# Kernel tuning notes

Measured on AMD Instinct MI355X. Metric: run time of the kernel, lower is better.

The kernel has to match this reference:

```python
import jax, jax.numpy as jnp
import numpy as np


def _unpack_int4(packed):
    """Unpack bytes (stored as int32 in [0,256)) into signed int4 values in [-8,7].
    packed: [..., K/2] -> [..., K], low nibble first."""
    lo = packed & 0xF
    hi = (packed >> 4) & 0xF
    lo = lo - 16 * (lo >= 8).astype(jnp.int32)
    hi = hi - 16 * (hi >= 8).astype(jnp.int32)
    out = jnp.stack([lo, hi], axis=-1)
    return out.reshape(packed.shape[:-1] + (packed.shape[-1] * 2,))


def setup_inputs() -> dict:
    key = jax.random.key(0)
    ks = jax.random.split(key, 7)
    M, K, N, R = 8192, 4096, 4096, 32
    return {
        "x_quant": jax.random.randint(ks[0], (M, K // 2), 0, 256, dtype=jnp.int32),
        "x_scale": jax.random.uniform(ks[1], (M,), dtype=jnp.float32) * 0.01 + 1e-3,
        "weight": jax.random.randint(ks[2], (N, K // 2), 0, 256, dtype=jnp.int32),
        "weight_scales": jax.random.uniform(ks[3], (N,), dtype=jnp.float32) * 0.01 + 1e-3,
        "bias": jax.random.normal(ks[4], (N,), dtype=jnp.float32) * 0.01,
        "x_r": jax.random.normal(ks[5], (M, R), dtype=jnp.float32),
        "w_outlier": jax.random.normal(ks[6], (N, R), dtype=jnp.float32),
    }


def reference(x_quant, x_scale, weight, weight_scales, bias, x_r, w_outlier):
    # Unpack packed int4 operands: [M,K] and [N,K], values in [-8,7]
    xq = _unpack_int4(x_quant)
    wq = _unpack_int4(weight)
    # Integer GEMM (s4s4 accumulate in int32), then fused dequant + bias
    acc = jnp.matmul(xq, wq.T)  # [M, N] int32
    out = acc.astype(jnp.float32) * x_scale[:, None] * weight_scales[None, :] + bias[None, :]
    # Low-rank outlier correction: addmm_(x_r, w_outlier.T)
    out = out + jnp.matmul(x_r, w_outlier.T)
    return out
```

## Files before the change

### kernel.cpp

```cpp
#include <hip/hip_runtime.h>

#define M_ 8192
#define K_ 4096
#define N_ 4096
#define R_ 32
#define KP_ (K_ / 2)

#define BM 256
#define BN 256
#define BK 64
#define NT (K_ / BK)
#define ATILE 16384
#define TILE_SZ 32768
#define GRID ((M_ / BM) * (N_ / BN))

typedef __attribute__((ext_vector_type(4))) int    i32x4;
typedef __attribute__((ext_vector_type(4))) float  f32x4;
typedef __attribute__((ext_vector_type(8))) __bf16 bf16x8;

__device__ __forceinline__ void gload16(const void* g, void* l) {
  __builtin_amdgcn_global_load_lds(
      (const __attribute__((address_space(1))) unsigned int*)g,
      (__attribute__((address_space(3))) unsigned int*)l, 16, 0, 0);
}

__device__ __forceinline__ unsigned nib2(int b) {
  unsigned lo = (unsigned)(((b & 15) ^ 8) - 8) & 0xFFu;
  unsigned hi = (unsigned)((((b >> 4) & 15) ^ 8) - 8) & 0xFFu;
  return lo | (hi << 8);
}

__global__ void repack_tiled(const int* __restrict__ in, uint4* __restrict__ out) {
  const int tile = blockIdx.x;
  const int rt = tile >> 6, kt = tile & 63;
  const int t = threadIdx.x;
  #pragma unroll
  for (int i = 0; i < 4; ++i) {
    int g = t + i * 256;
    int u = g >> 6, l = g & 63;
    int row = rt * 256 + u * 16 + (l & 15);
    int w0  = kt * 32 + (l >> 4) * 8;
    const int4* p = (const int4*)(in + (size_t)row * KP_ + w0);
    int4 a = p[0], b = p[1];
    uint4 o;
    o.x = nib2(a.x) | (nib2(a.y) << 16);
    o.y = nib2(a.z) | (nib2(a.w) << 16);
    o.z = nib2(b.x) | (nib2(b.y) << 16);
    o.w = nib2(b.z) | (nib2(b.w) << 16);
    out[(size_t)tile * 1024 + g] = o;
  }
}

__device__ __forceinline__ unsigned short f2b(float x) {
  unsigned u = __float_as_uint(x);
  return (unsigned short)((u + 0x7FFFu + ((u >> 16) & 1u)) >> 16);
}

__global__ void f2bf4(const float* __restrict__ in, unsigned short* __restrict__ out, int n4) {
  int stride = gridDim.x * blockDim.x;
  for (int i = blockIdx.x * blockDim.x + threadIdx.x; i < n4; i += stride) {
    float4 f = ((const float4*)in)[i];
    ushort4 o;
    o.x = f2b(f.x); o.y = f2b(f.y); o.z = f2b(f.z); o.w = f2b(f.w);
    ((ushort4*)out)[i] = o;
  }
}

__global__ __launch_bounds__(512, 2) void gemm_w4a4(
    const char* __restrict__ x8t, const char* __restrict__ w8t,
    const unsigned short* __restrict__ xrb, const unsigned short* __restrict__ wob,
    const float* __restrict__ xscale, const float* __restrict__ wscale,
    const float* __restrict__ bias, float* __restrict__ out)
{
  extern __shared__ __align__(16) char lds[];

  const int t    = threadIdx.x;
  const int w    = t >> 6;
  const int l    = t & 63;
  const int lrow = l & 15;
  const int lgrp = l >> 4;
  const int wr   = w >> 2;
  const int wc   = w & 3;

  const int swz = (blockIdx.x & 7) * (GRID / 8) + (blockIdx.x >> 3);
  const int mt  = swz & 31, nt = swz >> 5;
  const int m0  = mt * BM, n0 = nt * BN;

  const char* aT = x8t + (size_t)mt * NT * ATILE;
  const char* bT = w8t + (size_t)nt * NT * ATILE;

#define STAGE_A(tile)                                                         \
  { const char* s = aT + (size_t)(tile) * ATILE + w * 1024 + (l) * 16;        \
    char* d = lds + ((tile) & 3) * TILE_SZ + w * 1024;                        \
    gload16(s, d); gload16(s + 8192, d + 8192); }
#define STAGE_B(tile)                                                         \
  { const char* s = bT + (size_t)(tile) * ATILE + w * 1024 + (l) * 16;        \
    char* d = lds + ((tile) & 3) * TILE_SZ + ATILE + w * 1024;                \
    gload16(s, d); gload16(s + 8192, d + 8192); }
#define FENCE asm volatile("" ::: "memory")

  i32x4 acc[8][4] = {};

  STAGE_A(0) STAGE_B(0)
  STAGE_A(1) STAGE_B(1)
  STAGE_A(2) STAGE_B(2)
  asm volatile("s_waitcnt vmcnt(8)" ::: "memory");
  __builtin_amdgcn_s_barrier();
  FENCE;

  for (int kt = 0; kt < NT; ++kt) {
    const char* Ab = lds + (kt & 3) * TILE_SZ;
    const char* Bb = Ab + ATILE;

    i32x4 bf[4], af0[4];
    #pragma unroll
    for (int n = 0; n < 4; ++n)
      bf[n] = *(const i32x4*)(Bb + (wc * 4 + n) * 1024 + l * 16);
    #pragma unroll
    for (int m = 0; m < 4; ++m)
      af0[m] = *(const i32x4*)(Ab + (wr * 8 + m) * 1024 + l * 16);
    if (kt < NT - 3) STAGE_A(kt + 3)
    FENCE;
    __builtin_amdgcn_s_barrier();
    FENCE;
    __builtin_amdgcn_s_setprio(1);
    #pragma unroll
    for (int m = 0; m < 4; ++m)
      #pragma unroll
      for (int n = 0; n < 4; ++n)
        acc[m][n] = __builtin_amdgcn_mfma_i32_16x16x64_i8(af0[m], bf[n], acc[m][n], 0, 0, 0);
    __builtin_amdgcn_s_setprio(0);
    FENCE;
    __builtin_amdgcn_s_barrier();
    FENCE;

    i32x4 af1[4];
    #pragma unroll
    for (int m = 0; m < 4; ++m)
      af1[m] = *(const i32x4*)(Ab + (wr * 8 + 4 + m) * 1024 + l * 16);
    if (kt < NT - 3) {
      STAGE_B(kt + 3)
      asm volatile("s_waitcnt vmcnt(8)" ::: "memory");
    } else if (kt == NT - 3) {
      asm volatile("s_waitcnt vmcnt(4)" ::: "memory");
    } else if (kt == NT - 2) {
      asm volatile("s_waitcnt vmcnt(0)" ::: "memory");
    }
    FENCE;
    __builtin_amdgcn_s_barrier();
    FENCE;
    __builtin_amdgcn_s_setprio(1);
    #pragma unroll
    for (int m = 0; m < 4; ++m)
      #pragma unroll
      for (int n = 0; n < 4; ++n)
        acc[4 + m][n] = __builtin_amdgcn_mfma_i32_16x16x64_i8(af1[m], bf[n], acc[4 + m][n], 0, 0, 0);
    __builtin_amdgcn_s_setprio(0);
    FENCE;
    __builtin_amdgcn_s_barrier();
    FENCE;
  }

  f32x4 sxv[8];
  #pragma unroll
  for (int m = 0; m < 8; ++m)
    sxv[m] = *(const f32x4*)(xscale + m0 + wr * 128 + m * 16 + lgrp * 4);
  float swv[4], bv[4];
  #pragma unroll
  for (int n = 0; n < 4; ++n) {
    int cg = n0 + wc * 64 + n * 16 + lrow;
    swv[n] = wscale[cg];
    bv[n]  = bias[cg];
  }
  bf16x8 ar[8], br[4];
  #pragma unroll
  for (int m = 0; m < 8; ++m)
    ar[m] = *(const bf16x8*)(xrb + (size_t)(m0 + wr * 128 + m * 16 + lrow) * R_ + lgrp * 8);
  #pragma unroll
  for (int n = 0; n < 4; ++n)
    br[n] = *(const bf16x8*)(wob + (size_t)(n0 + wc * 64 + n * 16 + lrow) * R_ + lgrp * 8);

  #pragma unroll
  for (int m = 0; m < 8; ++m) {
    #pragma unroll
    for (int n = 0; n < 4; ++n) {
      f32x4 z = {0.0f, 0.0f, 0.0f, 0.0f};
      f32x4 c = __builtin_amdgcn_mfma_f32_16x16x32_bf16(ar[m], br[n], z, 0, 0, 0);
      #pragma unroll
      for (int j = 0; j < 4; ++j) {
        int rg = m0 + wr * 128 + m * 16 + lgrp * 4 + j;
        int cg = n0 + wc * 64 + n * 16 + lrow;
        out[(size_t)rg * N_ + cg] =
            (float)acc[m][n][j] * sxv[m][j] * swv[n] + c[j] + bv[n];
      }
    }
  }
}

extern "C" void kernel_launch(void* const* d_in, const int* in_sizes, int n_in,
                              void* d_out, int out_size, void* d_ws, size_t ws_size,
                              hipStream_t stream) {
  const int*   x_quant   = (const int*)d_in[0];
  const float* x_scale   = (const float*)d_in[1];
  const int*   weight    = (const int*)d_in[2];
  const float* w_scales  = (const float*)d_in[3];
  const float* bias      = (const float*)d_in[4];
  const float* x_r       = (const float*)d_in[5];
  const float* w_outlier = (const float*)d_in[6];
  float* out = (float*)d_out;

  char* ws = (char*)d_ws;
  char*           x8t = ws;
  char*           w8t = ws + (size_t)M_ * K_;
  unsigned short* xrb = (unsigned short*)(ws + (size_t)M_ * K_ + (size_t)N_ * K_);
  unsigned short* wob = xrb + (size_t)M_ * R_;

  (void)hipFuncSetAttribute((const void*)gemm_w4a4,
                            hipFuncAttributeMaxDynamicSharedMemorySize,
                            4 * TILE_SZ);

  repack_tiled<<<(M_ / BM) * NT, 256, 0, stream>>>(x_quant, (uint4*)x8t);
  repack_tiled<<<(N_ / BN) * NT, 256, 0, stream>>>(weight,  (uint4*)w8t);
  f2bf4<<<256, 256, 0, stream>>>(x_r, xrb, M_ * R_ / 4);
  f2bf4<<<128, 256, 0, stream>>>(w_outlier, wob, N_ * R_ / 4);

  gemm_w4a4<<<GRID, 512, 4 * TILE_SZ, stream>>>(
      x8t, w8t, xrb, wob, x_scale, w_scales, bias, out);
}
```

Baseline: 170.1 us.

## Switch int8 GEMM to 256x128 tiles with 32x32x32 MFMA and triple buffering

Reworks the GEMM: block tile shrinks from 256x256 to 256x128 with 4 waves instead of 8, each wave computing a 128x64 subtile using 32x32x32 int8 MFMAs in place of 16x16x64. The repack kernels are rewritten to produce a 32-row fragment layout that matches the new MFMA operand format, and the LDS pipeline moves from a 4-stage split A/B staging to a 3-buffer scheme with one barrier per k-step. The epilogue is adapted to the 32x32 accumulator layout. This doubles the grid and lowers per-block LDS use, which may help occupancy and cut barrier overhead, but it lowers data reuse per block and increases global traffic for A.

After: 202.5 us. 1.19x slower.

```diff
diff --git a/kernel.cpp b/kernel.cpp
--- a/kernel.cpp
+++ b/kernel.cpp
@@ -7,16 +7,19 @@
 #define KP_ (K_ / 2)
 
 #define BM 256
-#define BN 256
+#define BN 128
 #define BK 64
-#define NT (K_ / BK)
-#define ATILE 16384
-#define TILE_SZ 32768
+#define NT 64
+#define A_TILE 16384
+#define B_TILE 8192
+#define BUF_SZ (A_TILE + B_TILE)
 #define GRID ((M_ / BM) * (N_ / BN))
 
-typedef __attribute__((ext_vector_type(4))) int    i32x4;
-typedef __attribute__((ext_vector_type(4))) float  f32x4;
-typedef __attribute__((ext_vector_type(8))) __bf16 bf16x8;
+typedef __attribute__((ext_vector_type(4)))  int    i32x4;
+typedef __attribute__((ext_vector_type(16))) int    i32x16;
+typedef __attribute__((ext_vector_type(4)))  float  f32x4;
+typedef __attribute__((ext_vector_type(16))) float  f32x16;
+typedef __attribute__((ext_vector_type(8)))  __bf16 bf16x8;
 
 __device__ __forceinline__ void gload16(const void* g, void* l) {
   __builtin_amdgcn_global_load_lds(
@@ -30,25 +33,38 @@
   return lo | (hi << 8);
 }
 
-__global__ void repack_tiled(const int* __restrict__ in, uint4* __restrict__ out) {
-  const int tile = blockIdx.x;
-  const int rt = tile >> 6, kt = tile & 63;
-  const int t = threadIdx.x;
-  #pragma unroll
-  for (int i = 0; i < 4; ++i) {
-    int g = t + i * 256;
-    int u = g >> 6, l = g & 63;
-    int row = rt * 256 + u * 16 + (l & 15);
-    int w0  = kt * 32 + (l >> 4) * 8;
-    const int4* p = (const int4*)(in + (size_t)row * KP_ + w0);
-    int4 a = p[0], b = p[1];
-    uint4 o;
-    o.x = nib2(a.x) | (nib2(a.y) << 16);
-    o.y = nib2(a.z) | (nib2(a.w) << 16);
-    o.z = nib2(b.x) | (nib2(b.y) << 16);
-    o.w = nib2(b.z) | (nib2(b.w) << 16);
-    out[(size_t)tile * 1024 + g] = o;
-  }
+__global__ void repack_a(const int* __restrict__ in, uint4* __restrict__ out) {
+  int i = blockIdx.x * 256 + threadIdx.x;
+  int l = i & 63;
+  int u = (i >> 6) & 15;
+  int tile = i >> 10;
+  int row = (tile >> 6) * 256 + (u >> 1) * 32 + (l & 31);
+  int w0  = (tile & 63) * 32 + (u & 1) * 16 + (l >> 5) * 8;
+  const int4* p = (const int4*)(in + (size_t)row * KP_ + w0);
+  int4 a = p[0], b = p[1];
+  uint4 o;
+  o.x = nib2(a.x) | (nib2(a.y) << 16);
+  o.y = nib2(a.z) | (nib2(a.w) << 16);
+  o.z = nib2(b.x) | (nib2(b.y) << 16);
+  o.w = nib2(b.z) | (nib2(b.w) << 16);
+  out[i] = o;
+}
+
+__global__ void repack_b(const int* __restrict__ in, uint4* __restrict__ out) {
+  int i = blockIdx.x * 256 + threadIdx.x;
+  int l = i & 63;
+  int u = (i >> 6) & 7;
+  int tile = i >> 9;
+  int row = (tile >> 6) * 128 + (u >> 1) * 32 + (l & 31);
+  int w0  = (tile & 63) * 32 + (u & 1) * 16 + (l >> 5) * 8;
+  const int4* p = (const int4*)(in + (size_t)row * KP_ + w0);
+  int4 a = p[0], b = p[1];
+  uint4 o;
+  o.x = nib2(a.x) | (nib2(a.y) << 16);
+  o.y = nib2(a.z) | (nib2(a.w) << 16);
+  o.z = nib2(b.x) | (nib2(b.y) << 16);
+  o.w = nib2(b.z) | (nib2(b.w) << 16);
+  out[i] = o;
 }
 
 __device__ __forceinline__ unsigned short f2b(float x) {
@@ -66,132 +82,123 @@
   }
 }
 
-__global__ __launch_bounds__(512, 2) void gemm_w4a4(
+__global__ __launch_bounds__(256, 2) void gemm_w4a4(
     const char* __restrict__ x8t, const char* __restrict__ w8t,
     const unsigned short* __restrict__ xrb, const unsigned short* __restrict__ wob,
     const float* __restrict__ xscale, const float* __restrict__ wscale,
     const float* __restrict__ bias, float* __restrict__ out)
 {
-  extern __shared__ __align__(16) char lds[];
-
-  const int t    = threadIdx.x;
-  const int w    = t >> 6;
-  const int l    = t & 63;
-  const int lrow = l & 15;
-  const int lgrp = l >> 4;
-  const int wr   = w >> 2;
-  const int wc   = w & 3;
+  __shared__ __align__(16) char lds[3 * BUF_SZ];
+
+  const int t  = threadIdx.x;
+  const int w  = t >> 6;
+  const int l  = t & 63;
+  const int lr = l & 31;
+  const int lh = l >> 5;
+
+  const int wr = w >> 1;
+  const int wc = w & 1;
 
   const int swz = (blockIdx.x & 7) * (GRID / 8) + (blockIdx.x >> 3);
-  const int mt  = swz & 31, nt = swz >> 5;
-  const int m0  = mt * BM, n0 = nt * BN;
-
-  const char* aT = x8t + (size_t)mt * NT * ATILE;
-  const char* bT = w8t + (size_t)nt * NT * ATILE;
-
-#define STAGE_A(tile)                                                         \
-  { const char* s = aT + (size_t)(tile) * ATILE + w * 1024 + (l) * 16;        \
-    char* d = lds + ((tile) & 3) * TILE_SZ + w * 1024;                        \
-    gload16(s, d); gload16(s + 8192, d + 8192); }
-#define STAGE_B(tile)                                                         \
-  { const char* s = bT + (size_t)(tile) * ATILE + w * 1024 + (l) * 16;        \
-    char* d = lds + ((tile) & 3) * TILE_SZ + ATILE + w * 1024;                \
-    gload16(s, d); gload16(s + 8192, d + 8192); }
+  const int mt = swz & 31, ntile = swz >> 5;
+  const int m0 = mt * BM, n0 = ntile * BN;
+
+  const char* aT = x8t + (size_t)mt * NT * A_TILE;
+  const char* bT = w8t + (size_t)ntile * NT * B_TILE;
+
+#define STAGE(tile, buf)                                                      \
+  { const char* sa = aT + (size_t)(tile) * A_TILE + (w << 10) + (l << 4);     \
+    char* da = lds + (buf) * BUF_SZ + (w << 10);                              \
+    gload16(sa, da);                gload16(sa + 4096, da + 4096);            \
+    gload16(sa + 8192, da + 8192); gload16(sa + 12288, da + 12288);           \
+    const char* sb = bT + (size_t)(tile) * B_TILE + (w << 10) + (l << 4);     \
+    char* db = lds + (buf) * BUF_SZ + A_TILE + (w << 10);                     \
+    gload16(sb, db); gload16(sb + 4096, db + 4096); }
 #define FENCE asm volatile("" ::: "memory")
 
-  i32x4 acc[8][4] = {};
-
-  STAGE_A(0) STAGE_B(0)
-  STAGE_A(1) STAGE_B(1)
-  STAGE_A(2) STAGE_B(2)
-  asm volatile("s_waitcnt vmcnt(8)" ::: "memory");
+  i32x16 acc[4][2] = {};
+
+  STAGE(0, 0)
+  STAGE(1, 1)
+  asm volatile("s_waitcnt vmcnt(6)" ::: "memory");
   __builtin_amdgcn_s_barrier();
   FENCE;
 
+  int cur = 0;
   for (int kt = 0; kt < NT; ++kt) {
-    const char* Ab = lds + (kt & 3) * TILE_SZ;
-    const char* Bb = Ab + ATILE;
-
-    i32x4 bf[4], af0[4];
-    #pragma unroll
-    for (int n = 0; n < 4; ++n)
-      bf[n] = *(const i32x4*)(Bb + (wc * 4 + n) * 1024 + l * 16);
-    #pragma unroll
-    for (int m = 0; m < 4; ++m)
-      af0[m] = *(const i32x4*)(Ab + (wr * 8 + m) * 1024 + l * 16);
-    if (kt < NT - 3) STAGE_A(kt + 3)
-    FENCE;
+    const char* Ab = lds + cur * BUF_SZ;
+    const char* Bb = Ab + A_TILE;
+
+    i32x4 af[4][2], bf[2][2];
+    #pragma unroll
+    for (int mi = 0; mi < 4; ++mi)
+      #pragma unroll
+      for (int ks = 0; ks < 2; ++ks)
+        af[mi][ks] = *(const i32x4*)(Ab + (((wr * 4 + mi) * 2 + ks) << 10) + (l << 4));
+    #pragma unroll
+    for (int ni = 0; ni < 2; ++ni)
+      #pragma unroll
+      for (int ks = 0; ks < 2; ++ks)
+        bf[ni][ks] = *(const i32x4*)(Bb + (((wc * 2 + ni) * 2 + ks) << 10) + (l << 4));
+
+    int nbuf = cur + 2; if (nbuf >= 3) nbuf -= 3;
+    if (kt < NT - 2) {
+      STAGE(kt + 2, nbuf)
+      asm volatile("s_waitcnt vmcnt(6)" ::: "memory");
+    } else {
+      asm volatile("s_waitcnt vmcnt(0)" ::: "memory");
+    }
     __builtin_amdgcn_s_barrier();
     FENCE;
+
     __builtin_amdgcn_s_setprio(1);
     #pragma unroll
-    for (int m = 0; m < 4; ++m)
-      #pragma unroll
-      for (int n = 0; n < 4; ++n)
-        acc[m][n] = __builtin_amdgcn_mfma_i32_16x16x64_i8(af0[m], bf[n], acc[m][n], 0, 0, 0);
+    for (int ks = 0; ks < 2; ++ks)
+      #pragma unroll
+      for (int mi = 0; mi < 4; ++mi)
+        #pragma unroll
+        for (int ni = 0; ni < 2; ++ni)
+          acc[mi][ni] = __builtin_amdgcn_mfma_i32_32x32x32_i8(
+              af[mi][ks], bf[ni][ks], acc[mi][ni], 0, 0, 0);
     __builtin_amdgcn_s_setprio(0);
-    FENCE;
-    __builtin_amdgcn_s_barrier();
-    FENCE;
-
-    i32x4 af1[4];
-    #pragma unroll
-    for (int m = 0; m < 4; ++m)
-      af1[m] = *(const i32x4*)(Ab + (wr * 8 + 4 + m) * 1024 + l * 16);
-    if (kt < NT - 3) {
-      STAGE_B(kt + 3)
-      asm volatile("s_waitcnt vmcnt(8)" ::: "memory");
-    } else if (kt == NT - 3) {
-      asm volatile("s_waitcnt vmcnt(4)" ::: "memory");
-    } else if (kt == NT - 2) {
-      asm volatile("s_waitcnt vmcnt(0)" ::: "memory");
-    }
-    FENCE;
-    __builtin_amdgcn_s_barrier();
-    FENCE;
-    __builtin_amdgcn_s_setprio(1);
-    #pragma unroll
-    for (int m = 0; m < 4; ++m)
-      #pragma unroll
-      for (int n = 0; n < 4; ++n)
-        acc[4 + m][n] = __builtin_amdgcn_mfma_i32_16x16x64_i8(af1[m], bf[n], acc[4 + m][n], 0, 0, 0);
-    __builtin_amdgcn_s_setprio(0);
-    FENCE;
-    __builtin_amdgcn_s_barrier();
-    FENCE;
-  }
-
-  f32x4 sxv[8];
+
+    cur = cur + 1; if (cur >= 3) cur -= 3;
+  }
+
+  bf16x8 br0[2], br1[2];
+  float swv[2], bv[2];
   #pragma unroll
-  for (int m = 0; m < 8; ++m)
-    sxv[m] = *(const f32x4*)(xscale + m0 + wr * 128 + m * 16 + lgrp * 4);
-  float swv[4], bv[4];
+  for (int ni = 0; ni < 2; ++ni) {
+    int cg = n0 + wc * 64 + ni * 32 + lr;
+    const unsigned short* pw = wob + (size_t)cg * R_;
+    br0[ni] = *(const bf16x8*)(pw + lh * 8);
+    br1[ni] = *(const bf16x8*)(pw + 16 + lh * 8);
+    swv[ni] = wscale[cg];
+    bv[ni]  = bias[cg];
+  }
+
   #pragma unroll
-  for (int n = 0; n < 4; ++n) {
-    int cg = n0 + wc * 64 + n * 16 + lrow;
-    swv[n] = wscale[cg];
-    bv[n]  = bias[cg];
-  }
-  bf16x8 ar[8], br[4];
-  #pragma unroll
-  for (int m = 0; m < 8; ++m)
-    ar[m] = *(const bf16x8*)(xrb + (size_t)(m0 + wr * 128 + m * 16 + lrow) * R_ + lgrp * 8);
-  #pragma unroll
-  for (int n = 0; n < 4; ++n)
-    br[n] = *(const bf16x8*)(wob + (size_t)(n0 + wc * 64 + n * 16 + lrow) * R_ + lgrp * 8);
-
-  #pragma unroll
-  for (int m = 0; m < 8; ++m) {
-    #pragma unroll
-    for (int n = 0; n < 4; ++n) {
-      f32x4 z = {0.0f, 0.0f, 0.0f, 0.0f};
-      f32x4 c = __builtin_amdgcn_mfma_f32_16x16x32_bf16(ar[m], br[n], z, 0, 0, 0);
-      #pragma unroll
-      for (int j = 0; j < 4; ++j) {
-        int rg = m0 + wr * 128 + m * 16 + lgrp * 4 + j;
-        int cg = n0 + wc * 64 + n * 16 + lrow;
-        out[(size_t)rg * N_ + cg] =
-            (float)acc[m][n][j] * sxv[m][j] * swv[n] + c[j] + bv[n];
+  for (int mi = 0; mi < 4; ++mi) {
+    const int rbase = m0 + wr * 128 + mi * 32;
+    f32x4 sxg[4];
+    #pragma unroll
+    for (int g = 0; g < 4; ++g)
+      sxg[g] = *(const f32x4*)(xscale + rbase + g * 8 + 4 * lh);
+    const unsigned short* px = xrb + (size_t)(rbase + lr) * R_;
+    bf16x8 ar0 = *(const bf16x8*)(px + lh * 8);
+    bf16x8 ar1 = *(const bf16x8*)(px + 16 + lh * 8);
+
+    #pragma unroll
+    for (int ni = 0; ni < 2; ++ni) {
+      f32x16 c = {};
+      c = __builtin_amdgcn_mfma_f32_32x32x16_bf16(ar0, br0[ni], c, 0, 0, 0);
+      c = __builtin_amdgcn_mfma_f32_32x32x16_bf16(ar1, br1[ni], c, 0, 0, 0);
+      const int cg = n0 + wc * 64 + ni * 32 + lr;
+      #pragma unroll
+      for (int r = 0; r < 16; ++r) {
+        int row = rbase + (r & 3) + 8 * (r >> 2) + 4 * lh;
+        out[(size_t)row * N_ + cg] =
+            (float)acc[mi][ni][r] * sxg[r >> 2][r & 3] * swv[ni] + c[r] + bv[ni];
       }
     }
   }
@@ -215,15 +222,11 @@
   unsigned short* xrb = (unsigned short*)(ws + (size_t)M_ * K_ + (size_t)N_ * K_);
   unsigned short* wob = xrb + (size_t)M_ * R_;
 
-  (void)hipFuncSetAttribute((const void*)gemm_w4a4,
-                            hipFuncAttributeMaxDynamicSharedMemorySize,
-                            4 * TILE_SZ);
-
-  repack_tiled<<<(M_ / BM) * NT, 256, 0, stream>>>(x_quant, (uint4*)x8t);
-  repack_tiled<<<(N_ / BN) * NT, 256, 0, stream>>>(weight,  (uint4*)w8t);
+  repack_a<<<(M_ * K_ / 16) / 256, 256, 0, stream>>>(x_quant, (uint4*)x8t);
+  repack_b<<<(N_ * K_ / 16) / 256, 256, 0, stream>>>(weight,  (uint4*)w8t);
   f2bf4<<<256, 256, 0, stream>>>(x_r, xrb, M_ * R_ / 4);
   f2bf4<<<128, 256, 0, stream>>>(w_outlier, wob, N_ * R_ / 4);
 
-  gemm_w4a4<<<GRID, 512, 4 * TILE_SZ, stream>>>(
+  gemm_w4a4<<<GRID, 256, 0, stream>>>(
       x8t, w8t, xrb, wob, x_scale, w_scales, bias, out);
 }
```
